# Optimization experiments

Measured on AMD Instinct MI355X. Metric: run time of the kernel, lower is better.

The kernel has to match this reference:

```python
import jax, jax.numpy as jnp
import numpy as np
from jax.scipy.special import logsumexp

N, T, C, H, V = 8, 512, 1024, 256, 32000


def _res_layer(x, W1, b1, W2, b2):
    # hmm-lm ResLayer: x + ReLU(Linear(ReLU(Linear(x))))
    return x + jax.nn.relu(jax.nn.relu(x @ W1.T + b1) @ W2.T + b2)


def setup_inputs() -> dict:
    key = jax.random.key(0)
    ks = jax.random.split(key, 12)
    g = lambda k, shape: jax.random.normal(k, shape, jnp.float32) * (1.0 / np.sqrt(shape[-1]))
    return {
        "text": jax.random.randint(ks[0], (N, T), 0, V),
        "start_emb": jax.random.normal(ks[1], (H,), jnp.float32),
        "start_lin_W": g(ks[2], (H, H)),
        "start_lin_b": jnp.zeros((H,), jnp.float32),
        "start_res_W1": g(ks[3], (2, H, H)),
        "start_res_b1": jnp.zeros((2, H), jnp.float32),
        "start_res_W2": g(ks[4], (2, H, H)),
        "start_res_b2": jnp.zeros((2, H), jnp.float32),
        "state_emb": g(ks[5], (C, H)),
        "next_state_emb": g(ks[6], (C, H)),
        "preterminal_emb": g(ks[7], (C, H)),
        "term_res_W1": g(ks[8], (2, H, H)),
        "term_res_b1": jnp.zeros((2, H), jnp.float32),
        "term_res_W2": g(ks[9], (2, H, H)),
        "term_res_b2": jnp.zeros((2, H), jnp.float32),
        "terminal_emb": g(ks[10], (V, H)),
    }


def reference(text, start_emb, start_lin_W, start_lin_b,
              start_res_W1, start_res_b1, start_res_W2, start_res_b2,
              state_emb, next_state_emb, preterminal_emb,
              term_res_W1, term_res_b1, term_res_W2, term_res_b2,
              terminal_emb):
    # --- start distribution: start_mlp(start_emb) @ next_state_emb.T (tie_start) ---
    fx = start_emb @ start_lin_W.T + start_lin_b
    for i in range(2):
        fx = _res_layer(fx, start_res_W1[i], start_res_b1[i], start_res_W2[i], start_res_b2[i])
    start = jax.nn.log_softmax(fx @ next_state_emb.T)            # [C]

    # --- transition: log_softmax(state_emb @ next_state_emb.T) ---
    transition = jax.nn.log_softmax(state_emb @ next_state_emb.T, axis=-1)  # [C, C]

    # --- emission: log_softmax(terminal_mlp(preterminal_emb) @ terminal_emb.T) ---
    ft = preterminal_emb
    for i in range(2):
        ft = _res_layer(ft, term_res_W1[i], term_res_b1[i], term_res_W2[i], term_res_b2[i])
    emission = jax.nn.log_softmax(ft @ terminal_emb.T, axis=-1)  # [C, V]
    emis_t = emission.T                                          # [V, C]

    # --- HMM forward (log-space) scan; evidence = logsumexp(alpha_T) summed over batch ---
    alpha0 = start[None, :] + emis_t[text[:, 0]]                 # [N, C]

    def step(alpha, x_t):
        # alpha: [N, C]; x_t: [N]
        a = logsumexp(alpha[:, :, None] + transition[None], axis=1) + emis_t[x_t]
        return a, None

    alpha_T, _ = jax.lax.scan(step, alpha0, text[:, 1:].T)       # time-major [T-1, N]
    evidence = logsumexp(alpha_T, axis=-1).sum()
    return evidence
```

## Files before the change

### kernel.cpp

```cpp
#include <hip/hip_runtime.h>
#include <stdint.h>
#include <stddef.h>

#define N_ 8
#define T_ 512
#define C_ 1024
#define H_ 256
#define V_ 32000
#define CW 32

#define OFF_START   0u
#define OFF_LSE     4096u
#define OFF_EVP     8192u
#define OFF_EA      16384u
#define OFF_FT      81920u
#define OFF_P       1130496u
#define OFF_PART    5324800u
#define OFF_EEXP    5849088u

typedef __attribute__((ext_vector_type(8))) short short8;
typedef __attribute__((ext_vector_type(4))) float floatx4;

__device__ __forceinline__ float dot4(float4 a, float4 b) {
  return a.x*b.x + a.y*b.y + a.z*b.z + a.w*b.w;
}

__device__ __forceinline__ unsigned short f2bf(float f) {
  unsigned u = __float_as_uint(f);
  unsigned r = u + 0x7fffu + ((u >> 16) & 1u);
  return (unsigned short)(r >> 16);
}

__device__ __forceinline__ unsigned pk_bf2(float x, float y) {
  return ((unsigned)f2bf(y) << 16) | (unsigned)f2bf(x);
}

__device__ __forceinline__ short8 pack8(float4 a, float4 b) {
  union { short8 s; unsigned u[4]; } r;
  r.u[0] = pk_bf2(a.x, a.y);
  r.u[1] = pk_bf2(a.z, a.w);
  r.u[2] = pk_bf2(b.x, b.y);
  r.u[3] = pk_bf2(b.z, b.w);
  return r.s;
}

__global__ __launch_bounds__(256) void k_start(
    const float* __restrict__ se, const float* __restrict__ lw, const float* __restrict__ lb,
    const float* __restrict__ W1, const float* __restrict__ b1,
    const float* __restrict__ W2, const float* __restrict__ b2,
    const float* __restrict__ nse, float* __restrict__ out_start)
{
  __shared__ float xs[H_], fx[H_], h1[H_];
  __shared__ float lg[C_];
  __shared__ float redk[4];
  int tid = threadIdx.x;
  xs[tid] = se[tid];
  __syncthreads();
  {
    float acc = lb[tid];
    const float4* wr = (const float4*)(lw + (size_t)tid*H_);
    for (int k = 0; k < H_/4; ++k) acc += dot4(wr[k], *(const float4*)&xs[k*4]);
    fx[tid] = acc;
  }
  __syncthreads();
  for (int L = 0; L < 2; ++L) {
    {
      float acc = b1[L*H_ + tid];
      const float4* wr = (const float4*)(W1 + (size_t)(L*H_ + tid)*H_);
      for (int k = 0; k < H_/4; ++k) acc += dot4(wr[k], *(const float4*)&fx[k*4]);
      h1[tid] = fmaxf(acc, 0.f);
    }
    __syncthreads();
    {
      float acc = b2[L*H_ + tid];
      const float4* wr = (const float4*)(W2 + (size_t)(L*H_ + tid)*H_);
      for (int k = 0; k < H_/4; ++k) acc += dot4(wr[k], *(const float4*)&h1[k*4]);
      fx[tid] += fmaxf(acc, 0.f);
    }
    __syncthreads();
  }
  float lmax = -1e30f;
  for (int r = 0; r < 4; ++r) {
    int cc = tid + r*256;
    float acc = 0.f;
    const float4* er = (const float4*)(nse + (size_t)cc*H_);
    for (int k = 0; k < H_/4; ++k) acc += dot4(er[k], *(const float4*)&fx[k*4]);
    lg[cc] = acc;
    lmax = fmaxf(lmax, acc);
  }
  for (int m = 32; m; m >>= 1) lmax = fmaxf(lmax, __shfl_xor(lmax, m, 64));
  if ((tid & 63) == 0) redk[tid >> 6] = lmax;
  __syncthreads();
  float M = fmaxf(fmaxf(redk[0], redk[1]), fmaxf(redk[2], redk[3]));
  __syncthreads();
  float ssum = 0.f;
  for (int r = 0; r < 4; ++r) ssum += __expf(lg[tid + r*256] - M);
  for (int m = 32; m; m >>= 1) ssum += __shfl_xor(ssum, m, 64);
  if ((tid & 63) == 0) redk[tid >> 6] = ssum;
  __syncthreads();
  float S = redk[0] + redk[1] + redk[2] + redk[3];
  float lse = M + __logf(S);
  for (int r = 0; r < 4; ++r) {
    int cc = tid + r*256;
    out_start[cc] = lg[cc] - lse;
  }
}

__global__ __launch_bounds__(256) void k_gemm_cc(
    const float* __restrict__ A, const float* __restrict__ B, float* __restrict__ Cout)
{
  __shared__ float As[64][69];
  __shared__ float Bs[64][69];
  int tid = threadIdx.x;
  int bi = blockIdx.y, bj = blockIdx.x;
  int sr = tid >> 2, sq = tid & 3;
  int tx = tid & 15, ty = tid >> 4;
  float acc[4][4] = {};
  for (int kb = 0; kb < H_; kb += 64) {
    __syncthreads();
    {
      const float* ar = A + (size_t)(bi*64 + sr)*H_ + kb + sq*16;
      const float* br = B + (size_t)(bj*64 + sr)*H_ + kb + sq*16;
#pragma unroll
      for (int qq = 0; qq < 4; ++qq) {
        float4 av = *(const float4*)(ar + qq*4);
        float4 bv = *(const float4*)(br + qq*4);
        int kk = sq*16 + qq*4;
        As[sr][kk+0]=av.x; As[sr][kk+1]=av.y; As[sr][kk+2]=av.z; As[sr][kk+3]=av.w;
        Bs[sr][kk+0]=bv.x; Bs[sr][kk+1]=bv.y; Bs[sr][kk+2]=bv.z; Bs[sr][kk+3]=bv.w;
      }
    }
    __syncthreads();
#pragma unroll 4
    for (int k = 0; k < 64; ++k) {
      float a0 = As[ty*4+0][k], a1 = As[ty*4+1][k], a2 = As[ty*4+2][k], a3 = As[ty*4+3][k];
      float b0 = Bs[tx*4+0][k], b1 = Bs[tx*4+1][k], b2 = Bs[tx*4+2][k], b3 = Bs[tx*4+3][k];
      acc[0][0]+=a0*b0; acc[0][1]+=a0*b1; acc[0][2]+=a0*b2; acc[0][3]+=a0*b3;
      acc[1][0]+=a1*b0; acc[1][1]+=a1*b1; acc[1][2]+=a1*b2; acc[1][3]+=a1*b3;
      acc[2][0]+=a2*b0; acc[2][1]+=a2*b1; acc[2][2]+=a2*b2; acc[2][3]+=a2*b3;
      acc[3][0]+=a3*b0; acc[3][1]+=a3*b1; acc[3][2]+=a3*b2; acc[3][3]+=a3*b3;
    }
  }
#pragma unroll
  for (int ii = 0; ii < 4; ++ii)
#pragma unroll
    for (int jj = 0; jj < 4; ++jj)
      Cout[(size_t)(bi*64 + ty*4 + ii)*C_ + bj*64 + tx*4 + jj] = acc[ii][jj];
}

__global__ __launch_bounds__(256) void k_softmax_rows(float* __restrict__ P)
{
  __shared__ float redk[4];
  int row = blockIdx.x, tid = threadIdx.x;
  float4* pr = (float4*)(P + (size_t)row*C_);
  float4 v = pr[tid];
  float m = fmaxf(fmaxf(v.x, v.y), fmaxf(v.z, v.w));
  for (int mm = 32; mm; mm >>= 1) m = fmaxf(m, __shfl_xor(m, mm, 64));
  if ((tid & 63) == 0) redk[tid >> 6] = m;
  __syncthreads();
  float M = fmaxf(fmaxf(redk[0], redk[1]), fmaxf(redk[2], redk[3]));
  __syncthreads();
  float4 e;
  e.x = __expf(v.x - M); e.y = __expf(v.y - M); e.z = __expf(v.z - M); e.w = __expf(v.w - M);
  float s = e.x + e.y + e.z + e.w;
  for (int mm = 32; mm; mm >>= 1) s += __shfl_xor(s, mm, 64);
  if ((tid & 63) == 0) redk[tid >> 6] = s;
  __syncthreads();
  float S = redk[0] + redk[1] + redk[2] + redk[3];
  float inv = 1.0f / S;
  e.x *= inv; e.y *= inv; e.z *= inv; e.w *= inv;
  pr[tid] = e;
}

__global__ __launch_bounds__(256) void k_mlp(
    const float* __restrict__ inp, const float* __restrict__ W1, const float* __restrict__ b1,
    const float* __restrict__ W2, const float* __restrict__ b2, float* __restrict__ ft)
{
  __shared__ float xs[4][H_];
  __shared__ float hs[4][H_];
  int tid = threadIdx.x;
  int r0 = blockIdx.x * 4;
  int lr = tid >> 6, lc = (tid & 63) * 4;
  *(float4*)&xs[lr][lc] = *(const float4*)(inp + (size_t)(r0+lr)*H_ + lc);
  __syncthreads();
  for (int L = 0; L < 2; ++L) {
    {
      const float4* wr = (const float4*)(W1 + (size_t)(L*H_ + tid)*H_);
      float bb = b1[L*H_ + tid];
      float a0=bb, a1=bb, a2=bb, a3=bb;
      for (int k = 0; k < H_/4; ++k) {
        float4 w = wr[k];
        a0 += dot4(w, *(const float4*)&xs[0][k*4]);
        a1 += dot4(w, *(const float4*)&xs[1][k*4]);
        a2 += dot4(w, *(const float4*)&xs[2][k*4]);
        a3 += dot4(w, *(const float4*)&xs[3][k*4]);
      }
      hs[0][tid]=fmaxf(a0,0.f); hs[1][tid]=fmaxf(a1,0.f);
      hs[2][tid]=fmaxf(a2,0.f); hs[3][tid]=fmaxf(a3,0.f);
    }
    __syncthreads();
    {
      const float4* wr = (const float4*)(W2 + (size_t)(L*H_ + tid)*H_);
      float bb = b2[L*H_ + tid];
      float a0=bb, a1=bb, a2=bb, a3=bb;
      for (int k = 0; k < H_/4; ++k) {
        float4 w = wr[k];
        a0 += dot4(w, *(const float4*)&hs[0][k*4]);
        a1 += dot4(w, *(const float4*)&hs[1][k*4]);
        a2 += dot4(w, *(const float4*)&hs[2][k*4]);
        a3 += dot4(w, *(const float4*)&hs[3][k*4]);
      }
      xs[0][tid] += fmaxf(a0,0.f); xs[1][tid] += fmaxf(a1,0.f);
      xs[2][tid] += fmaxf(a2,0.f); xs[3][tid] += fmaxf(a3,0.f);
    }
    __syncthreads();
  }
  *(float4*)(ft + (size_t)(r0+lr)*H_ + lc) = *(float4*)&xs[lr][lc];
}

#define LSE_VSPLIT 16
#define LSE_VPB    2000
#define LSE_CHUNKS 125

__global__ __launch_bounds__(256) void k_lse_mfma(
    const float* __restrict__ ft, const float* __restrict__ emb, float* __restrict__ part)
{
  int tid = threadIdx.x;
  int lane = tid & 63;
  int w = tid >> 6;
  int q = blockIdx.x;
  int jb = blockIdx.y * 64 + w * 16;
  int r16 = lane & 15, kb = lane >> 4;

  short8 A[8];
  {
    const float* arow = ft + (size_t)(jb + r16) * H_ + kb * 8;
#pragma unroll
    for (int ks = 0; ks < 8; ++ks) {
      float4 a = *(const float4*)(arow + ks * 32);
      float4 b = *(const float4*)(arow + ks * 32 + 4);
      A[ks] = pack8(a, b);
    }
  }
  float s0 = 0.f, s1 = 0.f, s2 = 0.f, s3 = 0.f;
  const float* embq = emb + (size_t)q * LSE_VPB * H_;
#pragma unroll 1
  for (int ch = 0; ch < LSE_CHUNKS; ++ch) {
    const float* brow = embq + (size_t)(ch * 16 + r16) * H_ + kb * 8;
    floatx4 acca = {0,0,0,0}, accb = {0,0,0,0};
#pragma unroll
    for (int ks = 0; ks < 8; ks += 2) {
      float4 x0 = *(const float4*)(brow + ks * 32);
      float4 y0 = *(const float4*)(brow + ks * 32 + 4);
      float4 x1 = *(const float4*)(brow + ks * 32 + 32);
      float4 y1 = *(const float4*)(brow + ks * 32 + 36);
      acca = __builtin_amdgcn_mfma_f32_16x16x32_bf16(A[ks],   pack8(x0, y0), acca, 0, 0, 0);
      accb = __builtin_amdgcn_mfma_f32_16x16x32_bf16(A[ks+1], pack8(x1, y1), accb, 0, 0, 0);
    }
    s0 += __expf(acca[0] + accb[0]);
    s1 += __expf(acca[1] + accb[1]);
    s2 += __expf(acca[2] + accb[2]);
    s3 += __expf(acca[3] + accb[3]);
  }
#pragma unroll
  for (int mm = 1; mm <= 8; mm <<= 1) {
    s0 += __shfl_xor(s0, mm, 64);
    s1 += __shfl_xor(s1, mm, 64);
    s2 += __shfl_xor(s2, mm, 64);
    s3 += __shfl_xor(s3, mm, 64);
  }
  if (r16 == 0) {
    int jrow = jb + kb * 4;
    part[(size_t)(jrow + 0) * LSE_VSPLIT + q] = s0;
    part[(size_t)(jrow + 1) * LSE_VSPLIT + q] = s1;
    part[(size_t)(jrow + 2) * LSE_VSPLIT + q] = s2;
    part[(size_t)(jrow + 3) * LSE_VSPLIT + q] = s3;
  }
}

__global__ __launch_bounds__(256) void k_lse_reduce(
    const float* __restrict__ part, float* __restrict__ lse_row)
{
  int row = blockIdx.x * 256 + threadIdx.x;
  const float4* p = (const float4*)(part + (size_t)row * LSE_VSPLIT);
  float4 a = p[0], b = p[1], c = p[2], d = p[3];
  float s = a.x+a.y+a.z+a.w + b.x+b.y+b.z+b.w + c.x+c.y+c.z+c.w + d.x+d.y+d.z+d.w;
  lse_row[row] = __logf(s);
}

__global__ __launch_bounds__(256) void k_eexp_mfma(
    const float* __restrict__ ft, const float* __restrict__ emb, const int* __restrict__ text,
    const float* __restrict__ lse_row, float* __restrict__ EEXP)
{
  int tid = threadIdx.x;
  int lane = tid & 63;
  int w = tid >> 6;
  int jb = blockIdx.y * 64 + w * 16;
  int tb = blockIdx.x * 64;
  int r16 = lane & 15, kb = lane >> 4;

  short8 A[8];
  {
    const float* arow = ft + (size_t)(jb + r16) * H_ + kb * 8;
#pragma unroll
    for (int ks = 0; ks < 8; ++ks) {
      float4 a = *(const float4*)(arow + ks * 32);
      float4 b = *(const float4*)(arow + ks * 32 + 4);
      A[ks] = pack8(a, b);
    }
  }
  float4 lsej = *(const float4*)(lse_row + jb + kb * 4);

#pragma unroll 1
  for (int tc = 0; tc < 4; ++tc) {
    int idx = tb + tc * 16 + r16;
    int tok = text[idx];
    const float* brow = emb + (size_t)tok * H_ + kb * 8;
    floatx4 acca = {0,0,0,0}, accb = {0,0,0,0};
#pragma unroll
    for (int ks = 0; ks < 8; ks += 2) {
      float4 x0 = *(const float4*)(brow + ks * 32);
      float4 y0 = *(const float4*)(brow + ks * 32 + 4);
      float4 x1 = *(const float4*)(brow + ks * 32 + 32);
      float4 y1 = *(const float4*)(brow + ks * 32 + 36);
      acca = __builtin_amdgcn_mfma_f32_16x16x32_bf16(A[ks],   pack8(x0, y0), acca, 0, 0, 0);
      accb = __builtin_amdgcn_mfma_f32_16x16x32_bf16(A[ks+1], pack8(x1, y1), accb, 0, 0, 0);
    }
    float4 o;
    o.x = __expf(acca[0] + accb[0] - lsej.x);
    o.y = __expf(acca[1] + accb[1] - lsej.y);
    o.z = __expf(acca[2] + accb[2] - lsej.z);
    o.w = __expf(acca[3] + accb[3] - lsej.w);
    *(float4*)(EEXP + (size_t)idx * C_ + jb + kb * 4) = o;
  }
}

#define SCAN_LDS 71808

__global__ __launch_bounds__(256) void k_scan(
    const float* __restrict__ P, const float* __restrict__ EEXP, const float* __restrict__ startv,
    unsigned* __restrict__ eaG, float* __restrict__ evp)
{
  extern __shared__ char smem[];
  char*  Pl  = smem;
  char*  Bl  = smem + 65536;
  float* red = (float*)(smem + 69632);
  float* gmx = (float*)(smem + 71680);
  float* gmw = (float*)(smem + 71744);

  int tid  = threadIdx.x;
  int bid  = blockIdx.x;
  int c    = bid >> 2;
  int ng   = bid & 3;
  int n0   = ng * 2;
  int lane = tid & 63;
  int w    = tid >> 6;
  int seqh = lane >> 5;
  int kk   = lane & 31;

  if (tid < 64) {
    int s = tid >> 5, j = tid & 31;
    int col = c*CW + j;
    float val = __expf(startv[col]) * EEXP[((size_t)(n0+s)*T_ + 0)*C_ + col];
    unsigned word = ((unsigned)f2bf(val) << 16) | 1u;
    __hip_atomic_store(&eaG[(size_t)(0*N_ + n0+s)*C_ + col], word,
                       __ATOMIC_RELAXED, __HIP_MEMORY_SCOPE_AGENT);
  }

  {
    int j4 = (tid & 7) * 4;
    int irow = tid >> 3;
    for (int rep = 0; rep < 32; ++rep) {
      int i = rep*32 + irow;
      float4 v = *(const float4*)(P + (size_t)i*C_ + c*CW + j4);
      int ib = 2*i;
      *(unsigned short*)(Pl + (size_t)(j4+0)*2048 + (ib ^ (((j4+0)&7)<<4))) = f2bf(v.x);
      *(unsigned short*)(Pl + (size_t)(j4+1)*2048 + (ib ^ (((j4+1)&7)<<4))) = f2bf(v.y);
      *(unsigned short*)(Pl + (size_t)(j4+2)*2048 + (ib ^ (((j4+2)&7)<<4))) = f2bf(v.z);
      *(unsigned short*)(Pl + (size_t)(j4+3)*2048 + (ib ^ (((j4+3)&7)<<4))) = f2bf(v.w);
    }
  }
  __syncthreads();

  float ls0 = 0.f, ls1 = 0.f;

  int fidx = w*16 + (lane & 15);
  int fs   = fidx >> 5, fcol = fidx & 31;
  int j0 = lane & 15;
  const char* bp0 = Pl + (size_t)j0*2048;
  const char* bp1 = Pl + (size_t)(16+j0)*2048;
  int jswz = (j0 & 7) << 4;
  int ksub = lane >> 4;
  char* blw = Bl + w*1024;
  int arow = (lane & 15) & 1;

#pragma unroll 1
  for (int t = 1; t < T_; ++t) {
    int pprev = (t-1) & 1, pcur = t & 1;

    float eexp_reg = 0.f;
    if ((lane & 48) == 0 || lane < 16)
      eexp_reg = EEXP[((size_t)(n0+fs)*T_ + t)*C_ + c*CW + fcol];

    unsigned pend = 0xffu;
    float m = 0.f;
    floatx4 acc0 = {0,0,0,0}, acc1 = {0,0,0,0};
    unsigned tgt = (unsigned)t;
    unsigned* pbase = eaG + ((size_t)(pprev*N_ + n0+seqh)*C_ + w*256 + kk);
    int guard = 0;
    while (pend) {
      unsigned v[8];
      unsigned got = 0;
#pragma unroll
      for (int b = 0; b < 8; ++b) if (pend & (1u<<b))
        v[b] = __hip_atomic_load(pbase + b*32, __ATOMIC_RELAXED, __HIP_MEMORY_SCOPE_AGENT);
#pragma unroll
      for (int b = 0; b < 8; ++b) if (pend & (1u<<b)) {
        if (__ballot((v[b] & 0xffffu) == tgt) == ~0ull) got |= (1u<<b);
      }
      if (got) {
#pragma unroll
        for (int b = 0; b < 8; ++b) if (got & (1u<<b)) {
          m = fmaxf(m, __uint_as_float(v[b] & 0xffff0000u));
          *(unsigned short*)(blw + b*128 + seqh*64 + kk*2) = (unsigned short)(v[b] >> 16);
        }
        asm volatile("s_waitcnt lgkmcnt(0)" ::: "memory");
        __builtin_amdgcn_sched_barrier(0);
#pragma unroll
        for (int b = 0; b < 8; ++b) if (got & (1u<<b)) {
          short8 af = *(const short8*)(blw + b*128 + arow*64 + ksub*16);
          int kby = 2*(w*256 + b*32 + ksub*8);
          short8 b0 = *(const short8*)(bp0 + (kby ^ jswz));
          short8 b1 = *(const short8*)(bp1 + (kby ^ jswz));
          acc0 = __builtin_amdgcn_mfma_f32_16x16x32_bf16(af, b0, acc0, 0, 0, 0);
          acc1 = __builtin_amdgcn_mfma_f32_16x16x32_bf16(af, b1, acc1, 0, 0, 0);
        }
        pend &= ~got;
      } else {
        __builtin_amdgcn_s_sleep(1);
        if (++guard > 1000000) break;
      }
    }

#pragma unroll
    for (int mm = 1; mm <= 16; mm <<= 1) m = fmaxf(m, __shfl_xor(m, mm, 64));
    if (kk == 0) gmx[(pprev*4 + w)*2 + seqh] = m;

    if (lane < 16) {
      int rb = ((pprev*4 + w)*2)*2*16;
      red[rb +  0 + j0] = acc0[0];
      red[rb + 16 + j0] = acc0[1];
      red[rb + 32 + j0] = acc1[0];
      red[rb + 48 + j0] = acc1[1];
    }
    __syncthreads();

    float M0 = fmaxf(fmaxf(gmx[(pprev*4+0)*2+0], gmx[(pprev*4+1)*2+0]),
                     fmaxf(gmx[(pprev*4+2)*2+0], gmx[(pprev*4+3)*2+0]));
    float M1 = fmaxf(fmaxf(gmx[(pprev*4+0)*2+1], gmx[(pprev*4+1)*2+1]),
                     fmaxf(gmx[(pprev*4+2)*2+1], gmx[(pprev*4+3)*2+1]));
    ls0 += __logf(M0);
    ls1 += __logf(M1);

    if (lane < 16) {
      int tile = fcol >> 4, c16 = fcol & 15;
      float sum = 0.f;
#pragma unroll
      for (int ww = 0; ww < 4; ++ww)
        sum += red[(((pprev*4+ww)*2 + tile)*2 + fs)*16 + c16];
      float val = (sum / (fs ? M1 : M0)) * eexp_reg;
      unsigned word = ((unsigned)f2bf(val) << 16) | (unsigned)(t+1);
      __hip_atomic_store(&eaG[(size_t)(pcur*N_ + n0+fs)*C_ + c*CW + fcol], word,
                         __ATOMIC_RELAXED, __HIP_MEMORY_SCOPE_AGENT);
    }
  }

  if (c == 0) {
    const unsigned long long TMASK = 0x0000ffff0000ffffULL;
    {
      int sq = tid >> 7;
      int ib = (tid & 127) * 8;
      unsigned long long* src = (unsigned long long*)(eaG + ((size_t)(1*N_ + n0+sq)*C_ + ib));
      unsigned long long tpair = (unsigned long long)(unsigned)T_ | ((unsigned long long)(unsigned)T_ << 32);
      unsigned long long v0, v1, v2, v3;
      int guard = 0;
      for (;;) {
        v0 = __hip_atomic_load(src+0, __ATOMIC_RELAXED, __HIP_MEMORY_SCOPE_AGENT);
        v1 = __hip_atomic_load(src+1, __ATOMIC_RELAXED, __HIP_MEMORY_SCOPE_AGENT);
        v2 = __hip_atomic_load(src+2, __ATOMIC_RELAXED, __HIP_MEMORY_SCOPE_AGENT);
        v3 = __hip_atomic_load(src+3, __ATOMIC_RELAXED, __HIP_MEMORY_SCOPE_AGENT);
        bool ok = ((v0 & TMASK) == tpair) & ((v1 & TMASK) == tpair)
                & ((v2 & TMASK) == tpair) & ((v3 & TMASK) == tpair);
        if (ok) break;
        __builtin_amdgcn_s_sleep(1);
        if (++guard > 1000000) break;
      }
      float s8 = __uint_as_float((unsigned)v0       & 0xffff0000u)
               + __uint_as_float((unsigned)(v0>>32) & 0xffff0000u)
               + __uint_as_float((unsigned)v1       & 0xffff0000u)
               + __uint_as_float((unsigned)(v1>>32) & 0xffff0000u)
               + __uint_as_float((unsigned)v2       & 0xffff0000u)
               + __uint_as_float((unsigned)(v2>>32) & 0xffff0000u)
               + __uint_as_float((unsigned)v3       & 0xffff0000u)
               + __uint_as_float((unsigned)(v3>>32) & 0xffff0000u);
#pragma unroll
      for (int mm = 32; mm; mm >>= 1) s8 += __shfl_xor(s8, mm, 64);
      if ((tid & 63) == 0) gmw[tid >> 6] = s8;
    }
    __syncthreads();
    if (tid == 0) {
      float S0 = gmw[0] + gmw[1];
      float S1 = gmw[2] + gmw[3];
      evp[n0]     = ls0 + __logf(S0);
      evp[n0 + 1] = ls1 + __logf(S1);
    }
  }
}

__global__ void k_final(const float* __restrict__ evp, float* __restrict__ out)
{
  if (threadIdx.x == 0) {
    float s = 0.f;
#pragma unroll
    for (int i = 0; i < N_; ++i) s += evp[i];
    out[0] = s;
  }
}

extern "C" void kernel_launch(void* const* d_in, const int* in_sizes, int n_in,
                              void* d_out, int out_size, void* d_ws, size_t ws_size,
                              hipStream_t stream)
{
  const int*   text      = (const int*)  d_in[0];
  const float* start_emb = (const float*)d_in[1];
  const float* slw       = (const float*)d_in[2];
  const float* slb       = (const float*)d_in[3];
  const float* sW1       = (const float*)d_in[4];
  const float* sb1       = (const float*)d_in[5];
  const float* sW2       = (const float*)d_in[6];
  const float* sb2       = (const float*)d_in[7];
  const float* state_emb = (const float*)d_in[8];
  const float* nse       = (const float*)d_in[9];
  const float* pre_emb   = (const float*)d_in[10];
  const float* tW1       = (const float*)d_in[11];
  const float* tb1       = (const float*)d_in[12];
  const float* tW2       = (const float*)d_in[13];
  const float* tb2       = (const float*)d_in[14];
  const float* term_emb  = (const float*)d_in[15];

  char* ws = (char*)d_ws;
  float*    w_start = (float*)   (ws + OFF_START);
  float*    w_lse   = (float*)   (ws + OFF_LSE);
  float*    w_evp   = (float*)   (ws + OFF_EVP);
  unsigned* w_ea    = (unsigned*)(ws + OFF_EA);
  float*    w_ft    = (float*)   (ws + OFF_FT);
  float*    w_P     = (float*)   (ws + OFF_P);
  float*    w_part  = (float*)   (ws + OFF_PART);
  float*    w_eexp  = (float*)   (ws + OFF_EEXP);

  (void)hipMemsetAsync(w_ea, 0, 2*N_*C_*sizeof(unsigned), stream);

  k_start<<<1, 256, 0, stream>>>(start_emb, slw, slb, sW1, sb1, sW2, sb2, nse, w_start);
  k_gemm_cc<<<dim3(16,16), 256, 0, stream>>>(state_emb, nse, w_P);
  k_softmax_rows<<<C_, 256, 0, stream>>>(w_P);
  k_mlp<<<C_/4, 256, 0, stream>>>(pre_emb, tW1, tb1, tW2, tb2, w_ft);
  k_lse_mfma<<<dim3(LSE_VSPLIT, 16), 256, 0, stream>>>(w_ft, term_emb, w_part);
  k_lse_reduce<<<4, 256, 0, stream>>>(w_part, w_lse);
  k_eexp_mfma<<<dim3(64, 16), 256, 0, stream>>>(w_ft, term_emb, text, w_lse, w_eexp);

  (void)hipFuncSetAttribute((const void*)k_scan, hipFuncAttributeMaxDynamicSharedMemorySize, SCAN_LDS);
  k_scan<<<128, 256, SCAN_LDS, stream>>>(w_P, w_eexp, w_start, w_ea, w_evp);
  k_final<<<1, 64, 0, stream>>>(w_evp, (float*)d_out);
}
```

Baseline: 1.759 ms.

## Widen scan column slice to 64 per block and halve scan grid

Each scan block now owns 64 transition columns instead of 32, holding a 128KB bf16 slice of the transition matrix in LDS and running four MFMA accumulators per step. The grid shrinks from 128 to 64 blocks, so fewer blocks publish and poll the shared alpha buffer in the cross-block per-timestep handshake. The aim is to cut synchronisation and polling overhead per step. The cost is more compute per block on the serial critical path, fewer CUs in use, and a much larger LDS footprint.

```diff
diff --git a/kernel.cpp b/kernel.cpp
--- a/kernel.cpp
+++ b/kernel.cpp
@@ -7,7 +7,6 @@
 #define C_ 1024
 #define H_ 256
 #define V_ 32000
-#define CW 32
 
 #define OFF_START   0u
 #define OFF_LSE     4096u
@@ -335,7 +334,7 @@
   }
 }
 
-#define SCAN_LDS 71808
+#define SCAN_LDS 139344
 
 __global__ __launch_bounds__(256) void k_scan(
     const float* __restrict__ P, const float* __restrict__ EEXP, const float* __restrict__ startv,
@@ -343,24 +342,24 @@
 {
   extern __shared__ char smem[];
   char*  Pl  = smem;
-  char*  Bl  = smem + 65536;
-  float* red = (float*)(smem + 69632);
-  float* gmx = (float*)(smem + 71680);
-  float* gmw = (float*)(smem + 71744);
+  char*  Bl  = smem + 131072;
+  float* red = (float*)(smem + 135168);
+  float* gmx = (float*)(smem + 139264);
+  float* gmw = (float*)(smem + 139328);
 
   int tid  = threadIdx.x;
   int bid  = blockIdx.x;
-  int c    = bid >> 2;
-  int ng   = bid & 3;
+  int ng   = (bid & 7) >> 1;
+  int c    = ((bid >> 3) << 1) | (bid & 1);
   int n0   = ng * 2;
   int lane = tid & 63;
   int w    = tid >> 6;
   int seqh = lane >> 5;
   int kk   = lane & 31;
 
-  if (tid < 64) {
-    int s = tid >> 5, j = tid & 31;
-    int col = c*CW + j;
+  if (tid < 128) {
+    int s = tid >> 6, j = tid & 63;
+    int col = c*64 + j;
     float val = __expf(startv[col]) * EEXP[((size_t)(n0+s)*T_ + 0)*C_ + col];
     unsigned word = ((unsigned)f2bf(val) << 16) | 1u;
     __hip_atomic_store(&eaG[(size_t)(0*N_ + n0+s)*C_ + col], word,
@@ -368,43 +367,45 @@
   }
 
   {
-    int j4 = (tid & 7) * 4;
-    int irow = tid >> 3;
-    for (int rep = 0; rep < 32; ++rep) {
-      int i = rep*32 + irow;
-      float4 v = *(const float4*)(P + (size_t)i*C_ + c*CW + j4);
+    int j4 = (tid & 15) * 4;
+    int irow = tid >> 4;
+    for (int rep = 0; rep < 64; ++rep) {
+      int i = rep*16 + irow;
+      float4 v = *(const float4*)(P + (size_t)i*C_ + c*64 + j4);
       int ib = 2*i;
-      *(unsigned short*)(Pl + (size_t)(j4+0)*2048 + (ib ^ (((j4+0)&7)<<4))) = f2bf(v.x);
-      *(unsigned short*)(Pl + (size_t)(j4+1)*2048 + (ib ^ (((j4+1)&7)<<4))) = f2bf(v.y);
-      *(unsigned short*)(Pl + (size_t)(j4+2)*2048 + (ib ^ (((j4+2)&7)<<4))) = f2bf(v.z);
-      *(unsigned short*)(Pl + (size_t)(j4+3)*2048 + (ib ^ (((j4+3)&7)<<4))) = f2bf(v.w);
+      *(unsigned short*)(Pl + (size_t)(j4+0)*2048 + (ib ^ (((j4+0)&15)<<4))) = f2bf(v.x);
+      *(unsigned short*)(Pl + (size_t)(j4+1)*2048 + (ib ^ (((j4+1)&15)<<4))) = f2bf(v.y);
+      *(unsigned short*)(Pl + (size_t)(j4+2)*2048 + (ib ^ (((j4+2)&15)<<4))) = f2bf(v.z);
+      *(unsigned short*)(Pl + (size_t)(j4+3)*2048 + (ib ^ (((j4+3)&15)<<4))) = f2bf(v.w);
     }
   }
   __syncthreads();
 
   float ls0 = 0.f, ls1 = 0.f;
 
-  int fidx = w*16 + (lane & 15);
-  int fs   = fidx >> 5, fcol = fidx & 31;
+  int fidx = w*32 + (lane & 31);
+  int fs   = fidx >> 6, fcol = fidx & 63;
   int j0 = lane & 15;
   const char* bp0 = Pl + (size_t)j0*2048;
   const char* bp1 = Pl + (size_t)(16+j0)*2048;
-  int jswz = (j0 & 7) << 4;
+  const char* bp2 = Pl + (size_t)(32+j0)*2048;
+  const char* bp3 = Pl + (size_t)(48+j0)*2048;
+  int jswz = j0 << 4;
   int ksub = lane >> 4;
   char* blw = Bl + w*1024;
-  int arow = (lane & 15) & 1;
+  int arow = j0 & 1;
 
 #pragma unroll 1
   for (int t = 1; t < T_; ++t) {
     int pprev = (t-1) & 1, pcur = t & 1;
 
     float eexp_reg = 0.f;
-    if ((lane & 48) == 0 || lane < 16)
-      eexp_reg = EEXP[((size_t)(n0+fs)*T_ + t)*C_ + c*CW + fcol];
+    if (lane < 32)
+      eexp_reg = EEXP[((size_t)(n0+fs)*T_ + t)*C_ + c*64 + fcol];
 
     unsigned pend = 0xffu;
     float m = 0.f;
-    floatx4 acc0 = {0,0,0,0}, acc1 = {0,0,0,0};
+    floatx4 acc0 = {0,0,0,0}, acc1 = {0,0,0,0}, acc2 = {0,0,0,0}, acc3 = {0,0,0,0};
     unsigned tgt = (unsigned)t;
     unsigned* pbase = eaG + ((size_t)(pprev*N_ + n0+seqh)*C_ + w*256 + kk);
     int guard = 0;
@@ -430,10 +431,15 @@
         for (int b = 0; b < 8; ++b) if (got & (1u<<b)) {
           short8 af = *(const short8*)(blw + b*128 + arow*64 + ksub*16);
           int kby = 2*(w*256 + b*32 + ksub*8);
-          short8 b0 = *(const short8*)(bp0 + (kby ^ jswz));
-          short8 b1 = *(const short8*)(bp1 + (kby ^ jswz));
-          acc0 = __builtin_amdgcn_mfma_f32_16x16x32_bf16(af, b0, acc0, 0, 0, 0);
-          acc1 = __builtin_amdgcn_mfma_f32_16x16x32_bf16(af, b1, acc1, 0, 0, 0);
+          int ko = kby ^ jswz;
+          short8 f0 = *(const short8*)(bp0 + ko);
+          short8 f1 = *(const short8*)(bp1 + ko);
+          short8 f2 = *(const short8*)(bp2 + ko);
+          short8 f3 = *(const short8*)(bp3 + ko);
+          acc0 = __builtin_amdgcn_mfma_f32_16x16x32_bf16(af, f0, acc0, 0, 0, 0);
+          acc1 = __builtin_amdgcn_mfma_f32_16x16x32_bf16(af, f1, acc1, 0, 0, 0);
+          acc2 = __builtin_amdgcn_mfma_f32_16x16x32_bf16(af, f2, acc2, 0, 0, 0);
+          acc3 = __builtin_amdgcn_mfma_f32_16x16x32_bf16(af, f3, acc3, 0, 0, 0);
         }
         pend &= ~got;
       } else {
@@ -447,11 +453,11 @@
     if (kk == 0) gmx[(pprev*4 + w)*2 + seqh] = m;
 
     if (lane < 16) {
-      int rb = ((pprev*4 + w)*2)*2*16;
-      red[rb +  0 + j0] = acc0[0];
-      red[rb + 16 + j0] = acc0[1];
-      red[rb + 32 + j0] = acc1[0];
-      red[rb + 48 + j0] = acc1[1];
+      int rb = (pprev*4 + w)*128;
+      red[rb +   0 + j0] = acc0[0];  red[rb +  16 + j0] = acc0[1];
+      red[rb +  32 + j0] = acc1[0];  red[rb +  48 + j0] = acc1[1];
+      red[rb +  64 + j0] = acc2[0];  red[rb +  80 + j0] = acc2[1];
+      red[rb +  96 + j0] = acc3[0];  red[rb + 112 + j0] = acc3[1];
     }
     __syncthreads();
 
@@ -462,15 +468,15 @@
     ls0 += __logf(M0);
     ls1 += __logf(M1);
 
-    if (lane < 16) {
+    if (lane < 32) {
       int tile = fcol >> 4, c16 = fcol & 15;
       float sum = 0.f;
 #pragma unroll
       for (int ww = 0; ww < 4; ++ww)
-        sum += red[(((pprev*4+ww)*2 + tile)*2 + fs)*16 + c16];
+        sum += red[(pprev*4+ww)*128 + tile*32 + fs*16 + c16];
       float val = (sum / (fs ? M1 : M0)) * eexp_reg;
       unsigned word = ((unsigned)f2bf(val) << 16) | (unsigned)(t+1);
-      __hip_atomic_store(&eaG[(size_t)(pcur*N_ + n0+fs)*C_ + c*CW + fcol], word,
+      __hip_atomic_store(&eaG[(size_t)(pcur*N_ + n0+fs)*C_ + c*64 + fcol], word,
                          __ATOMIC_RELAXED, __HIP_MEMORY_SCOPE_AGENT);
     }
   }
@@ -569,6 +575,6 @@
   k_eexp_mfma<<<dim3(64, 16), 256, 0, stream>>>(w_ft, term_emb, text, w_lse, w_eexp);
 
   (void)hipFuncSetAttribute((const void*)k_scan, hipFuncAttributeMaxDynamicSharedMemorySize, SCAN_LDS);
-  k_scan<<<128, 256, SCAN_LDS, stream>>>(w_P, w_eexp, w_start, w_ea, w_evp);
+  k_scan<<<64, 256, SCAN_LDS, stream>>>(w_P, w_eexp, w_start, w_ea, w_evp);
   k_final<<<1, 64, 0, stream>>>(w_evp, (float*)d_out);
 }
```

New measurement: 1.903 ms. 1.08x slower.

## Give each wave a full sequence-half column slice to remove per-step block barrier

Applied to the files above, without the earlier changes.

Work inside the scan block is repartitioned so each wave owns one sequence and one 16-column half and reduces over the full 1024-length K dimension itself. This removes the per-timestep LDS reduction across waves and the __syncthreads. Each lane polls 8 contiguous 64-bit words for the previous alpha, and the waves proceed independently. In exchange every wave reads the whole alpha vector and issues 32 MFMAs per step instead of 8-16, so per-wave latency rises while block-level synchronization disappears. The LDS swizzle is widened to 16 rows to match the new access pattern.

```diff
diff --git a/kernel.cpp b/kernel.cpp
--- a/kernel.cpp
+++ b/kernel.cpp
@@ -335,18 +335,15 @@
   }
 }
 
-#define SCAN_LDS 71808
+#define SCAN_LDS (65536 + 8192)
 
 __global__ __launch_bounds__(256) void k_scan(
     const float* __restrict__ P, const float* __restrict__ EEXP, const float* __restrict__ startv,
     unsigned* __restrict__ eaG, float* __restrict__ evp)
 {
   extern __shared__ char smem[];
-  char*  Pl  = smem;
-  char*  Bl  = smem + 65536;
-  float* red = (float*)(smem + 69632);
-  float* gmx = (float*)(smem + 71680);
-  float* gmw = (float*)(smem + 71744);
+  char* Pl = smem;
+  char* Bl = smem + 65536;
 
   int tid  = threadIdx.x;
   int bid  = blockIdx.x;
@@ -355,15 +352,16 @@
   int n0   = ng * 2;
   int lane = tid & 63;
   int w    = tid >> 6;
-  int seqh = lane >> 5;
-  int kk   = lane & 31;
+  int sq   = w >> 1;
+  int h    = w & 1;
+  int seq  = n0 + sq;
 
   if (tid < 64) {
-    int s = tid >> 5, j = tid & 31;
+    int s0i = tid >> 5, j = tid & 31;
     int col = c*CW + j;
-    float val = __expf(startv[col]) * EEXP[((size_t)(n0+s)*T_ + 0)*C_ + col];
+    float val = __expf(startv[col]) * EEXP[((size_t)(n0+s0i)*T_ + 0)*C_ + col];
     unsigned word = ((unsigned)f2bf(val) << 16) | 1u;
-    __hip_atomic_store(&eaG[(size_t)(0*N_ + n0+s)*C_ + col], word,
+    __hip_atomic_store(&eaG[(size_t)(0*N_ + n0+s0i)*C_ + col], word,
                        __ATOMIC_RELAXED, __HIP_MEMORY_SCOPE_AGENT);
   }
 
@@ -374,68 +372,86 @@
       int i = rep*32 + irow;
       float4 v = *(const float4*)(P + (size_t)i*C_ + c*CW + j4);
       int ib = 2*i;
-      *(unsigned short*)(Pl + (size_t)(j4+0)*2048 + (ib ^ (((j4+0)&7)<<4))) = f2bf(v.x);
-      *(unsigned short*)(Pl + (size_t)(j4+1)*2048 + (ib ^ (((j4+1)&7)<<4))) = f2bf(v.y);
-      *(unsigned short*)(Pl + (size_t)(j4+2)*2048 + (ib ^ (((j4+2)&7)<<4))) = f2bf(v.z);
-      *(unsigned short*)(Pl + (size_t)(j4+3)*2048 + (ib ^ (((j4+3)&7)<<4))) = f2bf(v.w);
-    }
-  }
-  __syncthreads();
-
-  float ls0 = 0.f, ls1 = 0.f;
-
-  int fidx = w*16 + (lane & 15);
-  int fs   = fidx >> 5, fcol = fidx & 31;
-  int j0 = lane & 15;
-  const char* bp0 = Pl + (size_t)j0*2048;
-  const char* bp1 = Pl + (size_t)(16+j0)*2048;
-  int jswz = (j0 & 7) << 4;
-  int ksub = lane >> 4;
-  char* blw = Bl + w*1024;
-  int arow = (lane & 15) & 1;
+      *(unsigned short*)(Pl + (size_t)(j4+0)*2048 + (ib ^ (((j4+0)&15)<<4))) = f2bf(v.x);
+      *(unsigned short*)(Pl + (size_t)(j4+1)*2048 + (ib ^ (((j4+1)&15)<<4))) = f2bf(v.y);
+      *(unsigned short*)(Pl + (size_t)(j4+2)*2048 + (ib ^ (((j4+2)&15)<<4))) = f2bf(v.z);
+      *(unsigned short*)(Pl + (size_t)(j4+3)*2048 + (ib ^ (((j4+3)&15)<<4))) = f2bf(v.w);
+    }
+  }
+  __syncthreads();
+
+  float ls = 0.f;
+  const unsigned long long TMASK = 0x0000ffff0000ffffULL;
+
+  int myb  = lane >> 1;
+  int half = lane & 1;
+  int j0   = lane & 15;
+  int col  = h*16 + j0;
+  const char* bp = Pl + (size_t)col * 2048;
+  int jswz = j0 << 4;
+  int ks16 = (lane >> 4) * 16;
+  char* bw = Bl + w*2048;
+  int fcol = c*CW + h*16 + j0;
+  unsigned long long* psrc0 =
+      (unsigned long long*)(eaG + (size_t)seq*C_) + (size_t)myb*16 + half*8;
+  unsigned long long* psrc1 =
+      (unsigned long long*)(eaG + (size_t)(N_ + seq)*C_) + (size_t)myb*16 + half*8;
 
 #pragma unroll 1
   for (int t = 1; t < T_; ++t) {
     int pprev = (t-1) & 1, pcur = t & 1;
 
     float eexp_reg = 0.f;
-    if ((lane & 48) == 0 || lane < 16)
-      eexp_reg = EEXP[((size_t)(n0+fs)*T_ + t)*C_ + c*CW + fcol];
-
-    unsigned pend = 0xffu;
+    if (lane < 16)
+      eexp_reg = EEXP[((size_t)seq*T_ + t)*C_ + fcol];
+
+    unsigned long long* src = pprev ? psrc1 : psrc0;
+    unsigned long long tpair = (unsigned long long)(unsigned)t
+                             | ((unsigned long long)(unsigned)t << 32);
+
+    floatx4 acc = {0,0,0,0};
     float m = 0.f;
-    floatx4 acc0 = {0,0,0,0}, acc1 = {0,0,0,0};
-    unsigned tgt = (unsigned)t;
-    unsigned* pbase = eaG + ((size_t)(pprev*N_ + n0+seqh)*C_ + w*256 + kk);
+    unsigned long long pend = 0x5555555555555555ULL;
+    bool mydone = false;
     int guard = 0;
+
     while (pend) {
-      unsigned v[8];
-      unsigned got = 0;
-#pragma unroll
-      for (int b = 0; b < 8; ++b) if (pend & (1u<<b))
-        v[b] = __hip_atomic_load(pbase + b*32, __ATOMIC_RELAXED, __HIP_MEMORY_SCOPE_AGENT);
-#pragma unroll
-      for (int b = 0; b < 8; ++b) if (pend & (1u<<b)) {
-        if (__ballot((v[b] & 0xffffu) == tgt) == ~0ull) got |= (1u<<b);
+      if (!mydone) {
+        unsigned long long v[8];
+#pragma unroll
+        for (int j = 0; j < 8; ++j)
+          v[j] = __hip_atomic_load(src + j, __ATOMIC_RELAXED, __HIP_MEMORY_SCOPE_AGENT);
+        bool ok = true;
+#pragma unroll
+        for (int j = 0; j < 8; ++j) ok &= ((v[j] & TMASK) == tpair);
+        if (ok) {
+          unsigned pk[8];
+#pragma unroll
+          for (int j = 0; j < 8; ++j) {
+            unsigned lo = (unsigned)v[j], hi = (unsigned)(v[j] >> 32);
+            m = fmaxf(m, fmaxf(__uint_as_float(lo & 0xffff0000u),
+                               __uint_as_float(hi & 0xffff0000u)));
+            pk[j] = (lo >> 16) | (hi & 0xffff0000u);
+          }
+          *(uint4*)(bw + myb*64 + half*32)      = *(const uint4*)&pk[0];
+          *(uint4*)(bw + myb*64 + half*32 + 16) = *(const uint4*)&pk[4];
+          mydone = true;
+        }
       }
-      if (got) {
-#pragma unroll
-        for (int b = 0; b < 8; ++b) if (got & (1u<<b)) {
-          m = fmaxf(m, __uint_as_float(v[b] & 0xffff0000u));
-          *(unsigned short*)(blw + b*128 + seqh*64 + kk*2) = (unsigned short)(v[b] >> 16);
-        }
+      unsigned long long bal = __ballot(mydone);
+      unsigned long long rdy = bal & (bal >> 1) & 0x5555555555555555ULL;
+      unsigned long long newm = rdy & pend;
+      if (newm) {
         asm volatile("s_waitcnt lgkmcnt(0)" ::: "memory");
         __builtin_amdgcn_sched_barrier(0);
 #pragma unroll
-        for (int b = 0; b < 8; ++b) if (got & (1u<<b)) {
-          short8 af = *(const short8*)(blw + b*128 + arow*64 + ksub*16);
-          int kby = 2*(w*256 + b*32 + ksub*8);
-          short8 b0 = *(const short8*)(bp0 + (kby ^ jswz));
-          short8 b1 = *(const short8*)(bp1 + (kby ^ jswz));
-          acc0 = __builtin_amdgcn_mfma_f32_16x16x32_bf16(af, b0, acc0, 0, 0, 0);
-          acc1 = __builtin_amdgcn_mfma_f32_16x16x32_bf16(af, b1, acc1, 0, 0, 0);
+        for (int b = 0; b < 32; ++b) if ((newm >> (2*b)) & 1) {
+          short8 af = *(const short8*)(bw + b*64 + ks16);
+          int off = (b*64 + ks16) ^ jswz;
+          short8 bf = *(const short8*)(bp + off);
+          acc = __builtin_amdgcn_mfma_f32_16x16x32_bf16(af, bf, acc, 0, 0, 0);
         }
-        pend &= ~got;
+        pend &= ~newm;
       } else {
         __builtin_amdgcn_s_sleep(1);
         if (++guard > 1000000) break;
@@ -443,77 +459,42 @@
     }
 
 #pragma unroll
-    for (int mm = 1; mm <= 16; mm <<= 1) m = fmaxf(m, __shfl_xor(m, mm, 64));
-    if (kk == 0) gmx[(pprev*4 + w)*2 + seqh] = m;
+    for (int mm = 1; mm <= 32; mm <<= 1) m = fmaxf(m, __shfl_xor(m, mm, 64));
+    ls += __logf(m);
 
     if (lane < 16) {
-      int rb = ((pprev*4 + w)*2)*2*16;
-      red[rb +  0 + j0] = acc0[0];
-      red[rb + 16 + j0] = acc0[1];
-      red[rb + 32 + j0] = acc1[0];
-      red[rb + 48 + j0] = acc1[1];
-    }
-    __syncthreads();
-
-    float M0 = fmaxf(fmaxf(gmx[(pprev*4+0)*2+0], gmx[(pprev*4+1)*2+0]),
-                     fmaxf(gmx[(pprev*4+2)*2+0], gmx[(pprev*4+3)*2+0]));
-    float M1 = fmaxf(fmaxf(gmx[(pprev*4+0)*2+1], gmx[(pprev*4+1)*2+1]),
-                     fmaxf(gmx[(pprev*4+2)*2+1], gmx[(pprev*4+3)*2+1]));
-    ls0 += __logf(M0);
-    ls1 += __logf(M1);
-
-    if (lane < 16) {
-      int tile = fcol >> 4, c16 = fcol & 15;
-      float sum = 0.f;
-#pragma unroll
-      for (int ww = 0; ww < 4; ++ww)
-        sum += red[(((pprev*4+ww)*2 + tile)*2 + fs)*16 + c16];
-      float val = (sum / (fs ? M1 : M0)) * eexp_reg;
+      float val = (acc[0] / m) * eexp_reg;
       unsigned word = ((unsigned)f2bf(val) << 16) | (unsigned)(t+1);
-      __hip_atomic_store(&eaG[(size_t)(pcur*N_ + n0+fs)*C_ + c*CW + fcol], word,
+      __hip_atomic_store(&eaG[(size_t)(pcur*N_ + seq)*C_ + fcol], word,
                          __ATOMIC_RELAXED, __HIP_MEMORY_SCOPE_AGENT);
     }
   }
 
-  if (c == 0) {
-    const unsigned long long TMASK = 0x0000ffff0000ffffULL;
-    {
-      int sq = tid >> 7;
-      int ib = (tid & 127) * 8;
-      unsigned long long* src = (unsigned long long*)(eaG + ((size_t)(1*N_ + n0+sq)*C_ + ib));
-      unsigned long long tpair = (unsigned long long)(unsigned)T_ | ((unsigned long long)(unsigned)T_ << 32);
-      unsigned long long v0, v1, v2, v3;
-      int guard = 0;
-      for (;;) {
-        v0 = __hip_atomic_load(src+0, __ATOMIC_RELAXED, __HIP_MEMORY_SCOPE_AGENT);
-        v1 = __hip_atomic_load(src+1, __ATOMIC_RELAXED, __HIP_MEMORY_SCOPE_AGENT);
-        v2 = __hip_atomic_load(src+2, __ATOMIC_RELAXED, __HIP_MEMORY_SCOPE_AGENT);
-        v3 = __hip_atomic_load(src+3, __ATOMIC_RELAXED, __HIP_MEMORY_SCOPE_AGENT);
-        bool ok = ((v0 & TMASK) == tpair) & ((v1 & TMASK) == tpair)
-                & ((v2 & TMASK) == tpair) & ((v3 & TMASK) == tpair);
-        if (ok) break;
-        __builtin_amdgcn_s_sleep(1);
-        if (++guard > 1000000) break;
-      }
-      float s8 = __uint_as_float((unsigned)v0       & 0xffff0000u)
-               + __uint_as_float((unsigned)(v0>>32) & 0xffff0000u)
-               + __uint_as_float((unsigned)v1       & 0xffff0000u)
-               + __uint_as_float((unsigned)(v1>>32) & 0xffff0000u)
-               + __uint_as_float((unsigned)v2       & 0xffff0000u)
-               + __uint_as_float((unsigned)(v2>>32) & 0xffff0000u)
-               + __uint_as_float((unsigned)v3       & 0xffff0000u)
-               + __uint_as_float((unsigned)(v3>>32) & 0xffff0000u);
-#pragma unroll
-      for (int mm = 32; mm; mm >>= 1) s8 += __shfl_xor(s8, mm, 64);
-      if ((tid & 63) == 0) gmw[tid >> 6] = s8;
-    }
-    __syncthreads();
-    if (tid == 0) {
-      float S0 = gmw[0] + gmw[1];
-      float S1 = gmw[2] + gmw[3];
-      evp[n0]     = ls0 + __logf(S0);
-      evp[n0 + 1] = ls1 + __logf(S1);
-    }
+  if (c == 0 && h == 0) {
+    unsigned long long tpair = (unsigned long long)(unsigned)T_
+                             | ((unsigned long long)(unsigned)T_ << 32);
+    unsigned long long v[8];
+    int guard = 0;
+    for (;;) {
+#pragma unroll
+      for (int j = 0; j < 8; ++j)
+        v[j] = __hip_atomic_load(psrc1 + j, __ATOMIC_RELAXED, __HIP_MEMORY_SCOPE_AGENT);
+      bool ok = true;
+#pragma unroll
+      for (int j = 0; j < 8; ++j) ok &= ((v[j] & TMASK) == tpair);
+      if (__ballot(ok) == ~0ull) break;
+      __builtin_amdgcn_s_sleep(1);
+      if (++guard > 1000000) break;
+    }
+    float ssum = 0.f;
+#pragma unroll
+    for (int j = 0; j < 8; ++j) {
+      ssum += __uint_as_float((unsigned)v[j]        & 0xffff0000u);
+      ssum += __uint_as_float((unsigned)(v[j] >> 32) & 0xffff0000u);
+    }
+#pragma unroll
+    for (int mm = 1; mm <= 32; mm <<= 1) ssum += __shfl_xor(ssum, mm, 64);
+    if (lane == 0) evp[seq] = ls + __logf(ssum);
   }
 }
 
```

Measured after the change: 2.579 ms. 1.47x slower.
